# Optimization experiments

Hardware: AMD Instinct MI355X
Metric: run time of the kernel (lower is better)

## Reference

```python
import jax, jax.numpy as jnp
import numpy as np

N_STATE = 64   # n == m (required by the broadcast in the original forward)
SEQ_LEN = 200000


def setup_inputs() -> dict:
    key = jax.random.key(0)
    k_y, k_a, k_h = jax.random.split(key, 3)
    n = N_STATE
    # A scaled so spectral radius ~0.9 (stable recurrence), H ~ O(1) rows
    A = 0.9 * jax.random.normal(k_a, (n, n), dtype=jnp.float32) / jnp.sqrt(jnp.float32(n))
    H = jax.random.normal(k_h, (n, n), dtype=jnp.float32) / jnp.sqrt(jnp.float32(n))
    y = jax.random.normal(k_y, (n, SEQ_LEN), dtype=jnp.float32)
    L = jnp.float32(0.2)  # scalar learned gain (self.weights)
    return {"y": y, "A": A, "H": H, "L": L, "N": SEQ_LEN}


def reference(y, A, H, L, N):
    # x_{k+1} = A x_k + L * (y_k - H x_k);  yhat_k = H x_k  (pre-update state)
    # Vectorized over time with lax.scan (true sequential dependence).
    def step(x, yk):
        out = H @ x                      # [n] observation prediction at step k
        x_next = A @ x + L * (yk - out)  # [n] state update
        return x_next, out

    x0 = jnp.zeros((A.shape[0],), dtype=y.dtype)
    _, yhat_t = jax.lax.scan(step, x0, y.T)  # scan over time axis: y.T is [N, m]
    return yhat_t.T                          # [m, N]
```

## Files before the change

### kernel.cpp

```cpp
#include <hip/hip_runtime.h>


#define CHUNK 64
#define LOOKBACK 8

__global__ __launch_bounds__(1024) void kf_setup(const float* __restrict__ A,
                                                 const float* __restrict__ Hm,
                                                 const float* __restrict__ Lp,
                                                 float* __restrict__ ws) {
  __shared__ __align__(16) float s0[64 * 68];
  __shared__ __align__(16) float s1[64 * 68];
  const float Lg = Lp[0];
  const int t  = threadIdx.x;
  const int r  = t >> 4;
  const int c0 = (t & 15) * 4;

  {
    const float4 a4 = *(const float4*)(A  + r * 64 + c0);
    const float4 h4 = *(const float4*)(Hm + r * 64 + c0);
    float4 m4;
    m4.x = fmaf(-Lg, h4.x, a4.x);
    m4.y = fmaf(-Lg, h4.y, a4.y);
    m4.z = fmaf(-Lg, h4.z, a4.z);
    m4.w = fmaf(-Lg, h4.w, a4.w);
    *(float4*)(s0 + r * 68 + c0) = m4;
  }
  __syncthreads();

  float* src = s0;
  float* dst = s1;
  for (int sq = 0; sq < 6; ++sq) {
    float4 acc = make_float4(0.f, 0.f, 0.f, 0.f);
    const float* srow = src + r * 68;
    #pragma unroll 8
    for (int k = 0; k < 64; ++k) {
      const float  a  = srow[k];
      const float4 b4 = *(const float4*)(src + k * 68 + c0);
      acc.x = fmaf(a, b4.x, acc.x);
      acc.y = fmaf(a, b4.y, acc.y);
      acc.z = fmaf(a, b4.z, acc.z);
      acc.w = fmaf(a, b4.w, acc.w);
    }
    __syncthreads();
    *(float4*)(dst + r * 68 + c0) = acc;
    __syncthreads();
    float* tmp = src; src = dst; dst = tmp;
  }
  *(float4*)(ws + r * 64 + c0) = *(const float4*)(src + r * 68 + c0);
}

__global__ __launch_bounds__(64, 1) void kf_phase1(const float* __restrict__ y,
                                                   const float* __restrict__ A,
                                                   const float* __restrict__ Hm,
                                                   const float* __restrict__ Lp,
                                                   float* __restrict__ bvec,
                                                   int Nv) {
  const int c    = blockIdx.x;
  const int lane = threadIdx.x;
  const float Lg = Lp[0];
  __shared__ __align__(16) float xs[64];

  float Mrow[64];
  {
    const float* Ar = A  + lane * 64;
    const float* Hr = Hm + lane * 64;
    #pragma unroll
    for (int j = 0; j < 64; j += 4) {
      const float4 a4 = *(const float4*)(Ar + j);
      const float4 h4 = *(const float4*)(Hr + j);
      Mrow[j + 0] = fmaf(-Lg, h4.x, a4.x);
      Mrow[j + 1] = fmaf(-Lg, h4.y, a4.y);
      Mrow[j + 2] = fmaf(-Lg, h4.z, a4.z);
      Mrow[j + 3] = fmaf(-Lg, h4.w, a4.w);
    }
  }

  const int k0 = c * CHUNK;
  const float* yrow = y + (size_t)lane * (size_t)Nv + k0;
  const int nst = min(CHUNK, Nv - k0);
  float x = 0.f;

  if (nst == CHUNK) {
    #pragma unroll 1
    for (int t = 0; t < 4; ++t) {
      const float4 y0 = *(const float4*)(yrow + 16 * t + 0);
      const float4 y1 = *(const float4*)(yrow + 16 * t + 4);
      const float4 y2 = *(const float4*)(yrow + 16 * t + 8);
      const float4 y3 = *(const float4*)(yrow + 16 * t + 12);
      float yb[16];
      yb[0] = y0.x; yb[1] = y0.y; yb[2]  = y0.z; yb[3]  = y0.w;
      yb[4] = y1.x; yb[5] = y1.y; yb[6]  = y1.z; yb[7]  = y1.w;
      yb[8] = y2.x; yb[9] = y2.y; yb[10] = y2.z; yb[11] = y2.w;
      yb[12] = y3.x; yb[13] = y3.y; yb[14] = y3.z; yb[15] = y3.w;
      #pragma unroll
      for (int kk = 0; kk < 16; ++kk) {
        xs[lane] = x;
        __syncthreads();
        float a0 = 0.f, a1 = 0.f;
        #pragma unroll
        for (int jj = 0; jj < 16; ++jj) {
          const float4 xv = ((const float4*)xs)[jj];
          a0 = fmaf(Mrow[4 * jj + 0], xv.x, a0);
          a1 = fmaf(Mrow[4 * jj + 1], xv.y, a1);
          a0 = fmaf(Mrow[4 * jj + 2], xv.z, a0);
          a1 = fmaf(Mrow[4 * jj + 3], xv.w, a1);
        }
        __syncthreads();
        x = fmaf(Lg, yb[kk], a0 + a1);
      }
    }
  } else {
    for (int kk = 0; kk < nst; ++kk) {
      xs[lane] = x;
      __syncthreads();
      float a0 = 0.f, a1 = 0.f;
      #pragma unroll
      for (int jj = 0; jj < 16; ++jj) {
        const float4 xv = ((const float4*)xs)[jj];
        a0 = fmaf(Mrow[4 * jj + 0], xv.x, a0);
        a1 = fmaf(Mrow[4 * jj + 1], xv.y, a1);
        a0 = fmaf(Mrow[4 * jj + 2], xv.z, a0);
        a1 = fmaf(Mrow[4 * jj + 3], xv.w, a1);
      }
      __syncthreads();
      x = fmaf(Lg, yrow[kk], a0 + a1);
    }
  }
  bvec[c * 64 + lane] = x;
}

__global__ __launch_bounds__(64, 1) void kf_phase3(const float* __restrict__ y,
                                                   const float* __restrict__ A,
                                                   const float* __restrict__ Hm,
                                                   const float* __restrict__ Lp,
                                                   const float* __restrict__ bvec,
                                                   const float* __restrict__ P64,
                                                   float* __restrict__ out,
                                                   int Nv) {
  const int c    = blockIdx.x;
  const int lane = threadIdx.x;
  const float Lg = Lp[0];
  __shared__ __align__(16) float xs[64];

  float Mrow[64];
  {
    const float* Ar = A  + lane * 64;
    const float* Hr = Hm + lane * 64;
    #pragma unroll
    for (int j = 0; j < 64; j += 4) {
      const float4 a4 = *(const float4*)(Ar + j);
      const float4 h4 = *(const float4*)(Hr + j);
      Mrow[j + 0] = fmaf(-Lg, h4.x, a4.x);
      Mrow[j + 1] = fmaf(-Lg, h4.y, a4.y);
      Mrow[j + 2] = fmaf(-Lg, h4.z, a4.z);
      Mrow[j + 3] = fmaf(-Lg, h4.w, a4.w);
    }
  }

  float x = 0.f;
  {
    const int D = min(c, LOOKBACK);
    if (D > 0) {
      float Prow[64];
      #pragma unroll
      for (int j = 0; j < 64; j += 4) {
        const float4 p4 = *(const float4*)(P64 + lane * 64 + j);
        Prow[j + 0] = p4.x; Prow[j + 1] = p4.y;
        Prow[j + 2] = p4.z; Prow[j + 3] = p4.w;
      }
      x = bvec[(c - D) * 64 + lane];
      for (int t = D - 1; t >= 1; --t) {
        xs[lane] = x;
        __syncthreads();
        float a0 = 0.f, a1 = 0.f;
        #pragma unroll
        for (int jj = 0; jj < 16; ++jj) {
          const float4 xv = ((const float4*)xs)[jj];
          a0 = fmaf(Prow[4 * jj + 0], xv.x, a0);
          a1 = fmaf(Prow[4 * jj + 1], xv.y, a1);
          a0 = fmaf(Prow[4 * jj + 2], xv.z, a0);
          a1 = fmaf(Prow[4 * jj + 3], xv.w, a1);
        }
        __syncthreads();
        x = a0 + a1 + bvec[(c - t) * 64 + lane];
      }
    }
  }

  float Hrow[64];
  #pragma unroll
  for (int j = 0; j < 64; j += 4) {
    const float4 h4 = *(const float4*)(Hm + lane * 64 + j);
    Hrow[j + 0] = h4.x; Hrow[j + 1] = h4.y;
    Hrow[j + 2] = h4.z; Hrow[j + 3] = h4.w;
  }

  const int k0 = c * CHUNK;
  const float* yrow = y   + (size_t)lane * (size_t)Nv + k0;
  float*       orow = out + (size_t)lane * (size_t)Nv + k0;
  const int nst = min(CHUNK, Nv - k0);

  if (nst == CHUNK) {
    #pragma unroll 1
    for (int t = 0; t < 4; ++t) {
      const float4 y0 = *(const float4*)(yrow + 16 * t + 0);
      const float4 y1 = *(const float4*)(yrow + 16 * t + 4);
      const float4 y2 = *(const float4*)(yrow + 16 * t + 8);
      const float4 y3 = *(const float4*)(yrow + 16 * t + 12);
      float yb[16];
      yb[0] = y0.x; yb[1] = y0.y; yb[2]  = y0.z; yb[3]  = y0.w;
      yb[4] = y1.x; yb[5] = y1.y; yb[6]  = y1.z; yb[7]  = y1.w;
      yb[8] = y2.x; yb[9] = y2.y; yb[10] = y2.z; yb[11] = y2.w;
      yb[12] = y3.x; yb[13] = y3.y; yb[14] = y3.z; yb[15] = y3.w;

      float ob[16];
      #pragma unroll
      for (int kk = 0; kk < 16; ++kk) {
        xs[lane] = x;
        __syncthreads();
        float h0 = 0.f, h1 = 0.f, m0 = 0.f, m1 = 0.f;
        #pragma unroll
        for (int jj = 0; jj < 16; ++jj) {
          const float4 xv = ((const float4*)xs)[jj];
          h0 = fmaf(Hrow[4 * jj + 0], xv.x, h0);
          h1 = fmaf(Hrow[4 * jj + 1], xv.y, h1);
          m0 = fmaf(Mrow[4 * jj + 0], xv.x, m0);
          m1 = fmaf(Mrow[4 * jj + 1], xv.y, m1);
          h0 = fmaf(Hrow[4 * jj + 2], xv.z, h0);
          h1 = fmaf(Hrow[4 * jj + 3], xv.w, h1);
          m0 = fmaf(Mrow[4 * jj + 2], xv.z, m0);
          m1 = fmaf(Mrow[4 * jj + 3], xv.w, m1);
        }
        __syncthreads();
        ob[kk] = h0 + h1;
        x = fmaf(Lg, yb[kk], m0 + m1);
      }
      *(float4*)(orow + 16 * t + 0)  = make_float4(ob[0],  ob[1],  ob[2],  ob[3]);
      *(float4*)(orow + 16 * t + 4)  = make_float4(ob[4],  ob[5],  ob[6],  ob[7]);
      *(float4*)(orow + 16 * t + 8)  = make_float4(ob[8],  ob[9],  ob[10], ob[11]);
      *(float4*)(orow + 16 * t + 12) = make_float4(ob[12], ob[13], ob[14], ob[15]);
    }
  } else {
    for (int kk = 0; kk < nst; ++kk) {
      xs[lane] = x;
      __syncthreads();
      float h0 = 0.f, h1 = 0.f, m0 = 0.f, m1 = 0.f;
      #pragma unroll
      for (int jj = 0; jj < 16; ++jj) {
        const float4 xv = ((const float4*)xs)[jj];
        h0 = fmaf(Hrow[4 * jj + 0], xv.x, h0);
        h1 = fmaf(Hrow[4 * jj + 1], xv.y, h1);
        m0 = fmaf(Mrow[4 * jj + 0], xv.x, m0);
        m1 = fmaf(Mrow[4 * jj + 1], xv.y, m1);
        h0 = fmaf(Hrow[4 * jj + 2], xv.z, h0);
        h1 = fmaf(Hrow[4 * jj + 3], xv.w, h1);
        m0 = fmaf(Mrow[4 * jj + 2], xv.z, m0);
        m1 = fmaf(Mrow[4 * jj + 3], xv.w, m1);
      }
      __syncthreads();
      orow[kk] = h0 + h1;
      x = fmaf(Lg, yrow[kk], m0 + m1);
    }
  }
}

extern "C" void kernel_launch(void* const* d_in, const int* in_sizes, int n_in,
                              void* d_out, int out_size, void* d_ws, size_t ws_size,
                              hipStream_t stream) {
  const float* y  = (const float*)d_in[0];
  const float* A  = (const float*)d_in[1];
  const float* Hm = (const float*)d_in[2];
  const float* Lp = (const float*)d_in[3];
  const int Nv = in_sizes[0] / 64;
  const int P  = (Nv + CHUNK - 1) / CHUNK;

  float* ws   = (float*)d_ws;
  float* P64  = ws;
  float* bvec = ws + 4096;

  kf_setup<<<1, 1024, 0, stream>>>(A, Hm, Lp, P64);
  kf_phase1<<<P, 64, 0, stream>>>(y, A, Hm, Lp, bvec, Nv);
  kf_phase3<<<P, 64, 0, stream>>>(y, A, Hm, Lp, bvec, P64, (float*)d_out, Nv);
}
```

Before: 319.6 us.

## Batch several time chunks per block and zero-pad lookback to drop branches

Phase 1 now runs four independent chunks per 64-thread block and phase 3 runs two, packing their states into a float4 or float2 in shared memory. One barrier pair and one shared-memory read of the state then serve several chunks, which cuts the number of blocks and amortises synchronisation latency. The setup kernel zeros eight padding chunks ahead of the b-vector buffer, so the lookback always runs a fixed eight steps without a D<LOOKBACK branch. The partial-chunk tail path is gone, so correctness now depends on the sequence length being a multiple of the chunk size, and each step does more FMAs per thread.

```diff
diff --git a/kernel.cpp b/kernel.cpp
--- a/kernel.cpp
+++ b/kernel.cpp
@@ -14,6 +14,8 @@
   const int t  = threadIdx.x;
   const int r  = t >> 4;
   const int c0 = (t & 15) * 4;
+
+  if (t < 512) ws[4096 + t] = 0.f;
 
   {
     const float4 a4 = *(const float4*)(A  + r * 64 + c0);
@@ -53,12 +55,12 @@
                                                    const float* __restrict__ A,
                                                    const float* __restrict__ Hm,
                                                    const float* __restrict__ Lp,
-                                                   float* __restrict__ bvec,
-                                                   int Nv) {
-  const int c    = blockIdx.x;
+                                                   float* __restrict__ bb,
+                                                   int Nv, int P) {
   const int lane = threadIdx.x;
+  const int cb   = blockIdx.x * 4;
   const float Lg = Lp[0];
-  __shared__ __align__(16) float xs[64];
+  __shared__ __align__(16) float4 xs[64];
 
   float Mrow[64];
   {
@@ -75,72 +77,72 @@
     }
   }
 
-  const int k0 = c * CHUNK;
-  const float* yrow = y + (size_t)lane * (size_t)Nv + k0;
-  const int nst = min(CHUNK, Nv - k0);
-  float x = 0.f;
-
-  if (nst == CHUNK) {
-    #pragma unroll 1
-    for (int t = 0; t < 4; ++t) {
-      const float4 y0 = *(const float4*)(yrow + 16 * t + 0);
-      const float4 y1 = *(const float4*)(yrow + 16 * t + 4);
-      const float4 y2 = *(const float4*)(yrow + 16 * t + 8);
-      const float4 y3 = *(const float4*)(yrow + 16 * t + 12);
-      float yb[16];
-      yb[0] = y0.x; yb[1] = y0.y; yb[2]  = y0.z; yb[3]  = y0.w;
-      yb[4] = y1.x; yb[5] = y1.y; yb[6]  = y1.z; yb[7]  = y1.w;
-      yb[8] = y2.x; yb[9] = y2.y; yb[10] = y2.z; yb[11] = y2.w;
-      yb[12] = y3.x; yb[13] = y3.y; yb[14] = y3.z; yb[15] = y3.w;
+  const int c0 = min(cb + 0, P - 1);
+  const int c1 = min(cb + 1, P - 1);
+  const int c2 = min(cb + 2, P - 1);
+  const int c3 = min(cb + 3, P - 1);
+  const float* y0 = y + (size_t)lane * (size_t)Nv + c0 * CHUNK;
+  const float* y1 = y + (size_t)lane * (size_t)Nv + c1 * CHUNK;
+  const float* y2 = y + (size_t)lane * (size_t)Nv + c2 * CHUNK;
+  const float* y3 = y + (size_t)lane * (size_t)Nv + c3 * CHUNK;
+
+  float x0 = 0.f, x1 = 0.f, x2 = 0.f, x3 = 0.f;
+
+  #pragma unroll 1
+  for (int t = 0; t < 8; ++t) {
+    const float4 pa0 = *(const float4*)(y0 + 8 * t);
+    const float4 pb0 = *(const float4*)(y0 + 8 * t + 4);
+    const float4 pa1 = *(const float4*)(y1 + 8 * t);
+    const float4 pb1 = *(const float4*)(y1 + 8 * t + 4);
+    const float4 pa2 = *(const float4*)(y2 + 8 * t);
+    const float4 pb2 = *(const float4*)(y2 + 8 * t + 4);
+    const float4 pa3 = *(const float4*)(y3 + 8 * t);
+    const float4 pb3 = *(const float4*)(y3 + 8 * t + 4);
+    float yb0[8] = {pa0.x, pa0.y, pa0.z, pa0.w, pb0.x, pb0.y, pb0.z, pb0.w};
+    float yb1[8] = {pa1.x, pa1.y, pa1.z, pa1.w, pb1.x, pb1.y, pb1.z, pb1.w};
+    float yb2[8] = {pa2.x, pa2.y, pa2.z, pa2.w, pb2.x, pb2.y, pb2.z, pb2.w};
+    float yb3[8] = {pa3.x, pa3.y, pa3.z, pa3.w, pb3.x, pb3.y, pb3.z, pb3.w};
+
+    #pragma unroll
+    for (int kk = 0; kk < 8; ++kk) {
+      xs[lane] = make_float4(x0, x1, x2, x3);
+      __syncthreads();
+      float a0 = 0.f, a1 = 0.f, a2 = 0.f, a3 = 0.f;
       #pragma unroll
-      for (int kk = 0; kk < 16; ++kk) {
-        xs[lane] = x;
-        __syncthreads();
-        float a0 = 0.f, a1 = 0.f;
-        #pragma unroll
-        for (int jj = 0; jj < 16; ++jj) {
-          const float4 xv = ((const float4*)xs)[jj];
-          a0 = fmaf(Mrow[4 * jj + 0], xv.x, a0);
-          a1 = fmaf(Mrow[4 * jj + 1], xv.y, a1);
-          a0 = fmaf(Mrow[4 * jj + 2], xv.z, a0);
-          a1 = fmaf(Mrow[4 * jj + 3], xv.w, a1);
-        }
-        __syncthreads();
-        x = fmaf(Lg, yb[kk], a0 + a1);
+      for (int j = 0; j < 64; ++j) {
+        const float4 v = xs[j];
+        a0 = fmaf(Mrow[j], v.x, a0);
+        a1 = fmaf(Mrow[j], v.y, a1);
+        a2 = fmaf(Mrow[j], v.z, a2);
+        a3 = fmaf(Mrow[j], v.w, a3);
       }
-    }
-  } else {
-    for (int kk = 0; kk < nst; ++kk) {
-      xs[lane] = x;
-      __syncthreads();
-      float a0 = 0.f, a1 = 0.f;
-      #pragma unroll
-      for (int jj = 0; jj < 16; ++jj) {
-        const float4 xv = ((const float4*)xs)[jj];
-        a0 = fmaf(Mrow[4 * jj + 0], xv.x, a0);
-        a1 = fmaf(Mrow[4 * jj + 1], xv.y, a1);
-        a0 = fmaf(Mrow[4 * jj + 2], xv.z, a0);
-        a1 = fmaf(Mrow[4 * jj + 3], xv.w, a1);
-      }
-      __syncthreads();
-      x = fmaf(Lg, yrow[kk], a0 + a1);
-    }
-  }
-  bvec[c * 64 + lane] = x;
+      __syncthreads();
+      x0 = fmaf(Lg, yb0[kk], a0);
+      x1 = fmaf(Lg, yb1[kk], a1);
+      x2 = fmaf(Lg, yb2[kk], a2);
+      x3 = fmaf(Lg, yb3[kk], a3);
+    }
+  }
+  bb[c0 * 64 + lane] = x0;
+  bb[c1 * 64 + lane] = x1;
+  bb[c2 * 64 + lane] = x2;
+  bb[c3 * 64 + lane] = x3;
 }
 
 __global__ __launch_bounds__(64, 1) void kf_phase3(const float* __restrict__ y,
                                                    const float* __restrict__ A,
                                                    const float* __restrict__ Hm,
                                                    const float* __restrict__ Lp,
-                                                   const float* __restrict__ bvec,
+                                                   const float* __restrict__ bb,
                                                    const float* __restrict__ P64,
                                                    float* __restrict__ out,
-                                                   int Nv) {
-  const int c    = blockIdx.x;
+                                                   int Nv, int P) {
   const int lane = threadIdx.x;
+  const int cb   = blockIdx.x * 2;
+  const int c0   = min(cb + 0, P - 1);
+  const int c1   = min(cb + 1, P - 1);
   const float Lg = Lp[0];
-  __shared__ __align__(16) float xs[64];
+  __shared__ __align__(16) float2 xs[64];
 
   float Mrow[64];
   {
@@ -157,33 +159,33 @@
     }
   }
 
-  float x = 0.f;
-  {
-    const int D = min(c, LOOKBACK);
-    if (D > 0) {
-      float Prow[64];
+  float x0, x1;
+  {
+    float Prow[64];
+    #pragma unroll
+    for (int j = 0; j < 64; j += 4) {
+      const float4 p4 = *(const float4*)(P64 + lane * 64 + j);
+      Prow[j + 0] = p4.x; Prow[j + 1] = p4.y;
+      Prow[j + 2] = p4.z; Prow[j + 3] = p4.w;
+    }
+    x0 = bb[(c0 - LOOKBACK) * 64 + lane];
+    x1 = bb[(c1 - LOOKBACK) * 64 + lane];
+    #pragma unroll 1
+    for (int t = LOOKBACK - 1; t >= 1; --t) {
+      xs[lane] = make_float2(x0, x1);
+      __syncthreads();
+      float p0 = 0.f, p1 = 0.f, q0 = 0.f, q1 = 0.f;
       #pragma unroll
-      for (int j = 0; j < 64; j += 4) {
-        const float4 p4 = *(const float4*)(P64 + lane * 64 + j);
-        Prow[j + 0] = p4.x; Prow[j + 1] = p4.y;
-        Prow[j + 2] = p4.z; Prow[j + 3] = p4.w;
+      for (int jj = 0; jj < 32; ++jj) {
+        const float4 v = ((const float4*)xs)[jj];
+        p0 = fmaf(Prow[2 * jj + 0], v.x, p0);
+        p1 = fmaf(Prow[2 * jj + 0], v.y, p1);
+        q0 = fmaf(Prow[2 * jj + 1], v.z, q0);
+        q1 = fmaf(Prow[2 * jj + 1], v.w, q1);
       }
-      x = bvec[(c - D) * 64 + lane];
-      for (int t = D - 1; t >= 1; --t) {
-        xs[lane] = x;
-        __syncthreads();
-        float a0 = 0.f, a1 = 0.f;
-        #pragma unroll
-        for (int jj = 0; jj < 16; ++jj) {
-          const float4 xv = ((const float4*)xs)[jj];
-          a0 = fmaf(Prow[4 * jj + 0], xv.x, a0);
-          a1 = fmaf(Prow[4 * jj + 1], xv.y, a1);
-          a0 = fmaf(Prow[4 * jj + 2], xv.z, a0);
-          a1 = fmaf(Prow[4 * jj + 3], xv.w, a1);
-        }
-        __syncthreads();
-        x = a0 + a1 + bvec[(c - t) * 64 + lane];
-      }
+      __syncthreads();
+      x0 = p0 + q0 + bb[(c0 - t) * 64 + lane];
+      x1 = p1 + q1 + bb[(c1 - t) * 64 + lane];
     }
   }
 
@@ -195,72 +197,49 @@
     Hrow[j + 2] = h4.z; Hrow[j + 3] = h4.w;
   }
 
-  const int k0 = c * CHUNK;
-  const float* yrow = y   + (size_t)lane * (size_t)Nv + k0;
-  float*       orow = out + (size_t)lane * (size_t)Nv + k0;
-  const int nst = min(CHUNK, Nv - k0);
-
-  if (nst == CHUNK) {
-    #pragma unroll 1
-    for (int t = 0; t < 4; ++t) {
-      const float4 y0 = *(const float4*)(yrow + 16 * t + 0);
-      const float4 y1 = *(const float4*)(yrow + 16 * t + 4);
-      const float4 y2 = *(const float4*)(yrow + 16 * t + 8);
-      const float4 y3 = *(const float4*)(yrow + 16 * t + 12);
-      float yb[16];
-      yb[0] = y0.x; yb[1] = y0.y; yb[2]  = y0.z; yb[3]  = y0.w;
-      yb[4] = y1.x; yb[5] = y1.y; yb[6]  = y1.z; yb[7]  = y1.w;
-      yb[8] = y2.x; yb[9] = y2.y; yb[10] = y2.z; yb[11] = y2.w;
-      yb[12] = y3.x; yb[13] = y3.y; yb[14] = y3.z; yb[15] = y3.w;
-
-      float ob[16];
+  const float* yr0 = y   + (size_t)lane * (size_t)Nv + c0 * CHUNK;
+  const float* yr1 = y   + (size_t)lane * (size_t)Nv + c1 * CHUNK;
+  float*       o0  = out + (size_t)lane * (size_t)Nv + c0 * CHUNK;
+  float*       o1  = out + (size_t)lane * (size_t)Nv + c1 * CHUNK;
+
+  #pragma unroll 1
+  for (int t = 0; t < 8; ++t) {
+    const float4 pa0 = *(const float4*)(yr0 + 8 * t);
+    const float4 pb0 = *(const float4*)(yr0 + 8 * t + 4);
+    const float4 pa1 = *(const float4*)(yr1 + 8 * t);
+    const float4 pb1 = *(const float4*)(yr1 + 8 * t + 4);
+    float yb0[8] = {pa0.x, pa0.y, pa0.z, pa0.w, pb0.x, pb0.y, pb0.z, pb0.w};
+    float yb1[8] = {pa1.x, pa1.y, pa1.z, pa1.w, pb1.x, pb1.y, pb1.z, pb1.w};
+    float ob0[8], ob1[8];
+
+    #pragma unroll
+    for (int kk = 0; kk < 8; ++kk) {
+      xs[lane] = make_float2(x0, x1);
+      __syncthreads();
+      float h0e = 0.f, h1e = 0.f, m0e = 0.f, m1e = 0.f;
+      float h0o = 0.f, h1o = 0.f, m0o = 0.f, m1o = 0.f;
       #pragma unroll
-      for (int kk = 0; kk < 16; ++kk) {
-        xs[lane] = x;
-        __syncthreads();
-        float h0 = 0.f, h1 = 0.f, m0 = 0.f, m1 = 0.f;
-        #pragma unroll
-        for (int jj = 0; jj < 16; ++jj) {
-          const float4 xv = ((const float4*)xs)[jj];
-          h0 = fmaf(Hrow[4 * jj + 0], xv.x, h0);
-          h1 = fmaf(Hrow[4 * jj + 1], xv.y, h1);
-          m0 = fmaf(Mrow[4 * jj + 0], xv.x, m0);
-          m1 = fmaf(Mrow[4 * jj + 1], xv.y, m1);
-          h0 = fmaf(Hrow[4 * jj + 2], xv.z, h0);
-          h1 = fmaf(Hrow[4 * jj + 3], xv.w, h1);
-          m0 = fmaf(Mrow[4 * jj + 2], xv.z, m0);
-          m1 = fmaf(Mrow[4 * jj + 3], xv.w, m1);
-        }
-        __syncthreads();
-        ob[kk] = h0 + h1;
-        x = fmaf(Lg, yb[kk], m0 + m1);
+      for (int jj = 0; jj < 32; ++jj) {
+        const float4 v = ((const float4*)xs)[jj];
+        h0e = fmaf(Hrow[2 * jj + 0], v.x, h0e);
+        h1e = fmaf(Hrow[2 * jj + 0], v.y, h1e);
+        m0e = fmaf(Mrow[2 * jj + 0], v.x, m0e);
+        m1e = fmaf(Mrow[2 * jj + 0], v.y, m1e);
+        h0o = fmaf(Hrow[2 * jj + 1], v.z, h0o);
+        h1o = fmaf(Hrow[2 * jj + 1], v.w, h1o);
+        m0o = fmaf(Mrow[2 * jj + 1], v.z, m0o);
+        m1o = fmaf(Mrow[2 * jj + 1], v.w, m1o);
       }
-      *(float4*)(orow + 16 * t + 0)  = make_float4(ob[0],  ob[1],  ob[2],  ob[3]);
-      *(float4*)(orow + 16 * t + 4)  = make_float4(ob[4],  ob[5],  ob[6],  ob[7]);
-      *(float4*)(orow + 16 * t + 8)  = make_float4(ob[8],  ob[9],  ob[10], ob[11]);
-      *(float4*)(orow + 16 * t + 12) = make_float4(ob[12], ob[13], ob[14], ob[15]);
-    }
-  } else {
-    for (int kk = 0; kk < nst; ++kk) {
-      xs[lane] = x;
-      __syncthreads();
-      float h0 = 0.f, h1 = 0.f, m0 = 0.f, m1 = 0.f;
-      #pragma unroll
-      for (int jj = 0; jj < 16; ++jj) {
-        const float4 xv = ((const float4*)xs)[jj];
-        h0 = fmaf(Hrow[4 * jj + 0], xv.x, h0);
-        h1 = fmaf(Hrow[4 * jj + 1], xv.y, h1);
-        m0 = fmaf(Mrow[4 * jj + 0], xv.x, m0);
-        m1 = fmaf(Mrow[4 * jj + 1], xv.y, m1);
-        h0 = fmaf(Hrow[4 * jj + 2], xv.z, h0);
-        h1 = fmaf(Hrow[4 * jj + 3], xv.w, h1);
-        m0 = fmaf(Mrow[4 * jj + 2], xv.z, m0);
-        m1 = fmaf(Mrow[4 * jj + 3], xv.w, m1);
-      }
-      __syncthreads();
-      orow[kk] = h0 + h1;
-      x = fmaf(Lg, yrow[kk], m0 + m1);
-    }
+      __syncthreads();
+      ob0[kk] = h0e + h0o;
+      ob1[kk] = h1e + h1o;
+      x0 = fmaf(Lg, yb0[kk], m0e + m0o);
+      x1 = fmaf(Lg, yb1[kk], m1e + m1o);
+    }
+    *(float4*)(o0 + 8 * t)     = make_float4(ob0[0], ob0[1], ob0[2], ob0[3]);
+    *(float4*)(o0 + 8 * t + 4) = make_float4(ob0[4], ob0[5], ob0[6], ob0[7]);
+    *(float4*)(o1 + 8 * t)     = make_float4(ob1[0], ob1[1], ob1[2], ob1[3]);
+    *(float4*)(o1 + 8 * t + 4) = make_float4(ob1[4], ob1[5], ob1[6], ob1[7]);
   }
 }
 
@@ -276,9 +255,9 @@
 
   float* ws   = (float*)d_ws;
   float* P64  = ws;
-  float* bvec = ws + 4096;
-
-  kf_setup<<<1, 1024, 0, stream>>>(A, Hm, Lp, P64);
-  kf_phase1<<<P, 64, 0, stream>>>(y, A, Hm, Lp, bvec, Nv);
-  kf_phase3<<<P, 64, 0, stream>>>(y, A, Hm, Lp, bvec, P64, (float*)d_out, Nv);
-}
+  float* bb   = ws + 4096 + 512;
+
+  kf_setup<<<1, 1024, 0, stream>>>(A, Hm, Lp, ws);
+  kf_phase1<<<(P + 3) / 4, 64, 0, stream>>>(y, A, Hm, Lp, bb, Nv, P);
+  kf_phase3<<<(P + 1) / 2, 64, 0, stream>>>(y, A, Hm, Lp, bb, P64, (float*)d_out, Nv, P);
+}
```

Result: slower. 871.5 us (+172.7%).

## Replace LDS broadcast and barriers with readlane broadcasts in recurrence loops

Applied to the files above, without the earlier changes.

The per-step state broadcast now uses wave readlane intrinsics instead of an LDS store, two __syncthreads and LDS loads, since each block is a single 64-lane wavefront. Each step then runs as pure register/scalar work. The lookback branch is removed by zero-padding 8 chunks of bvec ahead of the real data, so every block runs a uniform lookback. Launch bounds are raised to allow more blocks per CU, and accumulation is split into four chains for more ILP. Readlane puts 64 scalar ops on the critical path of every step, and the higher occupancy target may cost registers.

```diff
diff --git a/kernel.cpp b/kernel.cpp
--- a/kernel.cpp
+++ b/kernel.cpp
@@ -3,6 +3,10 @@
 
 #define CHUNK 64
 #define LOOKBACK 8
+
+__device__ __forceinline__ float bcast(float x, int l) {
+  return __uint_as_float(__builtin_amdgcn_readlane(__float_as_uint(x), l));
+}
 
 __global__ __launch_bounds__(1024) void kf_setup(const float* __restrict__ A,
                                                  const float* __restrict__ Hm,
@@ -14,6 +18,8 @@
   const int t  = threadIdx.x;
   const int r  = t >> 4;
   const int c0 = (t & 15) * 4;
+
+  if (t < 512) ws[4096 + t] = 0.f;
 
   {
     const float4 a4 = *(const float4*)(A  + r * 64 + c0);
@@ -49,16 +55,15 @@
   *(float4*)(ws + r * 64 + c0) = *(const float4*)(src + r * 68 + c0);
 }
 
-__global__ __launch_bounds__(64, 1) void kf_phase1(const float* __restrict__ y,
+__global__ __launch_bounds__(64, 4) void kf_phase1(const float* __restrict__ y,
                                                    const float* __restrict__ A,
                                                    const float* __restrict__ Hm,
                                                    const float* __restrict__ Lp,
-                                                   float* __restrict__ bvec,
+                                                   float* __restrict__ bb,
                                                    int Nv) {
   const int c    = blockIdx.x;
   const int lane = threadIdx.x;
   const float Lg = Lp[0];
-  __shared__ __align__(16) float xs[64];
 
   float Mrow[64];
   {
@@ -82,65 +87,58 @@
 
   if (nst == CHUNK) {
     #pragma unroll 1
-    for (int t = 0; t < 4; ++t) {
-      const float4 y0 = *(const float4*)(yrow + 16 * t + 0);
-      const float4 y1 = *(const float4*)(yrow + 16 * t + 4);
-      const float4 y2 = *(const float4*)(yrow + 16 * t + 8);
-      const float4 y3 = *(const float4*)(yrow + 16 * t + 12);
-      float yb[16];
-      yb[0] = y0.x; yb[1] = y0.y; yb[2]  = y0.z; yb[3]  = y0.w;
-      yb[4] = y1.x; yb[5] = y1.y; yb[6]  = y1.z; yb[7]  = y1.w;
-      yb[8] = y2.x; yb[9] = y2.y; yb[10] = y2.z; yb[11] = y2.w;
-      yb[12] = y3.x; yb[13] = y3.y; yb[14] = y3.z; yb[15] = y3.w;
-      #pragma unroll
-      for (int kk = 0; kk < 16; ++kk) {
-        xs[lane] = x;
-        __syncthreads();
-        float a0 = 0.f, a1 = 0.f;
+    for (int t = 0; t < 8; ++t) {
+      const float4 p0 = *(const float4*)(yrow + 8 * t);
+      const float4 p1 = *(const float4*)(yrow + 8 * t + 4);
+      const float yb[8] = {p0.x, p0.y, p0.z, p0.w, p1.x, p1.y, p1.z, p1.w};
+      #pragma unroll
+      for (int kk = 0; kk < 8; ++kk) {
+        float a0 = 0.f, a1 = 0.f, a2 = 0.f, a3 = 0.f;
         #pragma unroll
-        for (int jj = 0; jj < 16; ++jj) {
-          const float4 xv = ((const float4*)xs)[jj];
-          a0 = fmaf(Mrow[4 * jj + 0], xv.x, a0);
-          a1 = fmaf(Mrow[4 * jj + 1], xv.y, a1);
-          a0 = fmaf(Mrow[4 * jj + 2], xv.z, a0);
-          a1 = fmaf(Mrow[4 * jj + 3], xv.w, a1);
+        for (int j = 0; j < 64; j += 4) {
+          const float s0 = bcast(x, j + 0);
+          const float s1 = bcast(x, j + 1);
+          const float s2 = bcast(x, j + 2);
+          const float s3 = bcast(x, j + 3);
+          a0 = fmaf(Mrow[j + 0], s0, a0);
+          a1 = fmaf(Mrow[j + 1], s1, a1);
+          a2 = fmaf(Mrow[j + 2], s2, a2);
+          a3 = fmaf(Mrow[j + 3], s3, a3);
         }
-        __syncthreads();
-        x = fmaf(Lg, yb[kk], a0 + a1);
+        x = fmaf(Lg, yb[kk], (a0 + a1) + (a2 + a3));
       }
     }
   } else {
     for (int kk = 0; kk < nst; ++kk) {
-      xs[lane] = x;
-      __syncthreads();
-      float a0 = 0.f, a1 = 0.f;
-      #pragma unroll
-      for (int jj = 0; jj < 16; ++jj) {
-        const float4 xv = ((const float4*)xs)[jj];
-        a0 = fmaf(Mrow[4 * jj + 0], xv.x, a0);
-        a1 = fmaf(Mrow[4 * jj + 1], xv.y, a1);
-        a0 = fmaf(Mrow[4 * jj + 2], xv.z, a0);
-        a1 = fmaf(Mrow[4 * jj + 3], xv.w, a1);
-      }
-      __syncthreads();
-      x = fmaf(Lg, yrow[kk], a0 + a1);
-    }
-  }
-  bvec[c * 64 + lane] = x;
-}
-
-__global__ __launch_bounds__(64, 1) void kf_phase3(const float* __restrict__ y,
+      float a0 = 0.f, a1 = 0.f, a2 = 0.f, a3 = 0.f;
+      #pragma unroll
+      for (int j = 0; j < 64; j += 4) {
+        const float s0 = bcast(x, j + 0);
+        const float s1 = bcast(x, j + 1);
+        const float s2 = bcast(x, j + 2);
+        const float s3 = bcast(x, j + 3);
+        a0 = fmaf(Mrow[j + 0], s0, a0);
+        a1 = fmaf(Mrow[j + 1], s1, a1);
+        a2 = fmaf(Mrow[j + 2], s2, a2);
+        a3 = fmaf(Mrow[j + 3], s3, a3);
+      }
+      x = fmaf(Lg, yrow[kk], (a0 + a1) + (a2 + a3));
+    }
+  }
+  bb[c * 64 + lane] = x;
+}
+
+__global__ __launch_bounds__(64, 2) void kf_phase3(const float* __restrict__ y,
                                                    const float* __restrict__ A,
                                                    const float* __restrict__ Hm,
                                                    const float* __restrict__ Lp,
-                                                   const float* __restrict__ bvec,
+                                                   const float* __restrict__ bb,
                                                    const float* __restrict__ P64,
                                                    float* __restrict__ out,
                                                    int Nv) {
   const int c    = blockIdx.x;
   const int lane = threadIdx.x;
   const float Lg = Lp[0];
-  __shared__ __align__(16) float xs[64];
 
   float Mrow[64];
   {
@@ -157,33 +155,31 @@
     }
   }
 
-  float x = 0.f;
-  {
-    const int D = min(c, LOOKBACK);
-    if (D > 0) {
-      float Prow[64];
+  float x;
+  {
+    float Prow[64];
+    #pragma unroll
+    for (int j = 0; j < 64; j += 4) {
+      const float4 p4 = *(const float4*)(P64 + lane * 64 + j);
+      Prow[j + 0] = p4.x; Prow[j + 1] = p4.y;
+      Prow[j + 2] = p4.z; Prow[j + 3] = p4.w;
+    }
+    x = bb[(c - LOOKBACK) * 64 + lane];
+    #pragma unroll 1
+    for (int t = LOOKBACK - 1; t >= 1; --t) {
+      float a0 = 0.f, a1 = 0.f, a2 = 0.f, a3 = 0.f;
       #pragma unroll
       for (int j = 0; j < 64; j += 4) {
-        const float4 p4 = *(const float4*)(P64 + lane * 64 + j);
-        Prow[j + 0] = p4.x; Prow[j + 1] = p4.y;
-        Prow[j + 2] = p4.z; Prow[j + 3] = p4.w;
-      }
-      x = bvec[(c - D) * 64 + lane];
-      for (int t = D - 1; t >= 1; --t) {
-        xs[lane] = x;
-        __syncthreads();
-        float a0 = 0.f, a1 = 0.f;
-        #pragma unroll
-        for (int jj = 0; jj < 16; ++jj) {
-          const float4 xv = ((const float4*)xs)[jj];
-          a0 = fmaf(Prow[4 * jj + 0], xv.x, a0);
-          a1 = fmaf(Prow[4 * jj + 1], xv.y, a1);
-          a0 = fmaf(Prow[4 * jj + 2], xv.z, a0);
-          a1 = fmaf(Prow[4 * jj + 3], xv.w, a1);
-        }
-        __syncthreads();
-        x = a0 + a1 + bvec[(c - t) * 64 + lane];
-      }
+        const float s0 = bcast(x, j + 0);
+        const float s1 = bcast(x, j + 1);
+        const float s2 = bcast(x, j + 2);
+        const float s3 = bcast(x, j + 3);
+        a0 = fmaf(Prow[j + 0], s0, a0);
+        a1 = fmaf(Prow[j + 1], s1, a1);
+        a2 = fmaf(Prow[j + 2], s2, a2);
+        a3 = fmaf(Prow[j + 3], s3, a3);
+      }
+      x = (a0 + a1) + (a2 + a3) + bb[(c - t) * 64 + lane];
     }
   }
 
@@ -202,64 +198,57 @@
 
   if (nst == CHUNK) {
     #pragma unroll 1
-    for (int t = 0; t < 4; ++t) {
-      const float4 y0 = *(const float4*)(yrow + 16 * t + 0);
-      const float4 y1 = *(const float4*)(yrow + 16 * t + 4);
-      const float4 y2 = *(const float4*)(yrow + 16 * t + 8);
-      const float4 y3 = *(const float4*)(yrow + 16 * t + 12);
-      float yb[16];
-      yb[0] = y0.x; yb[1] = y0.y; yb[2]  = y0.z; yb[3]  = y0.w;
-      yb[4] = y1.x; yb[5] = y1.y; yb[6]  = y1.z; yb[7]  = y1.w;
-      yb[8] = y2.x; yb[9] = y2.y; yb[10] = y2.z; yb[11] = y2.w;
-      yb[12] = y3.x; yb[13] = y3.y; yb[14] = y3.z; yb[15] = y3.w;
-
-      float ob[16];
-      #pragma unroll
-      for (int kk = 0; kk < 16; ++kk) {
-        xs[lane] = x;
-        __syncthreads();
-        float h0 = 0.f, h1 = 0.f, m0 = 0.f, m1 = 0.f;
+    for (int t = 0; t < 8; ++t) {
+      const float4 p0 = *(const float4*)(yrow + 8 * t);
+      const float4 p1 = *(const float4*)(yrow + 8 * t + 4);
+      const float yb[8] = {p0.x, p0.y, p0.z, p0.w, p1.x, p1.y, p1.z, p1.w};
+      float ob[8];
+      #pragma unroll
+      for (int kk = 0; kk < 8; ++kk) {
+        float h0 = 0.f, h1 = 0.f, h2 = 0.f, h3 = 0.f;
+        float m0 = 0.f, m1 = 0.f, m2 = 0.f, m3 = 0.f;
         #pragma unroll
-        for (int jj = 0; jj < 16; ++jj) {
-          const float4 xv = ((const float4*)xs)[jj];
-          h0 = fmaf(Hrow[4 * jj + 0], xv.x, h0);
-          h1 = fmaf(Hrow[4 * jj + 1], xv.y, h1);
-          m0 = fmaf(Mrow[4 * jj + 0], xv.x, m0);
-          m1 = fmaf(Mrow[4 * jj + 1], xv.y, m1);
-          h0 = fmaf(Hrow[4 * jj + 2], xv.z, h0);
-          h1 = fmaf(Hrow[4 * jj + 3], xv.w, h1);
-          m0 = fmaf(Mrow[4 * jj + 2], xv.z, m0);
-          m1 = fmaf(Mrow[4 * jj + 3], xv.w, m1);
+        for (int j = 0; j < 64; j += 4) {
+          const float s0 = bcast(x, j + 0);
+          const float s1 = bcast(x, j + 1);
+          const float s2 = bcast(x, j + 2);
+          const float s3 = bcast(x, j + 3);
+          h0 = fmaf(Hrow[j + 0], s0, h0);
+          m0 = fmaf(Mrow[j + 0], s0, m0);
+          h1 = fmaf(Hrow[j + 1], s1, h1);
+          m1 = fmaf(Mrow[j + 1], s1, m1);
+          h2 = fmaf(Hrow[j + 2], s2, h2);
+          m2 = fmaf(Mrow[j + 2], s2, m2);
+          h3 = fmaf(Hrow[j + 3], s3, h3);
+          m3 = fmaf(Mrow[j + 3], s3, m3);
         }
-        __syncthreads();
-        ob[kk] = h0 + h1;
-        x = fmaf(Lg, yb[kk], m0 + m1);
-      }
-      *(float4*)(orow + 16 * t + 0)  = make_float4(ob[0],  ob[1],  ob[2],  ob[3]);
-      *(float4*)(orow + 16 * t + 4)  = make_float4(ob[4],  ob[5],  ob[6],  ob[7]);
-      *(float4*)(orow + 16 * t + 8)  = make_float4(ob[8],  ob[9],  ob[10], ob[11]);
-      *(float4*)(orow + 16 * t + 12) = make_float4(ob[12], ob[13], ob[14], ob[15]);
+        ob[kk] = (h0 + h1) + (h2 + h3);
+        x = fmaf(Lg, yb[kk], (m0 + m1) + (m2 + m3));
+      }
+      *(float4*)(orow + 8 * t)     = make_float4(ob[0], ob[1], ob[2], ob[3]);
+      *(float4*)(orow + 8 * t + 4) = make_float4(ob[4], ob[5], ob[6], ob[7]);
     }
   } else {
     for (int kk = 0; kk < nst; ++kk) {
-      xs[lane] = x;
-      __syncthreads();
-      float h0 = 0.f, h1 = 0.f, m0 = 0.f, m1 = 0.f;
-      #pragma unroll
-      for (int jj = 0; jj < 16; ++jj) {
-        const float4 xv = ((const float4*)xs)[jj];
-        h0 = fmaf(Hrow[4 * jj + 0], xv.x, h0);
-        h1 = fmaf(Hrow[4 * jj + 1], xv.y, h1);
-        m0 = fmaf(Mrow[4 * jj + 0], xv.x, m0);
-        m1 = fmaf(Mrow[4 * jj + 1], xv.y, m1);
-        h0 = fmaf(Hrow[4 * jj + 2], xv.z, h0);
-        h1 = fmaf(Hrow[4 * jj + 3], xv.w, h1);
-        m0 = fmaf(Mrow[4 * jj + 2], xv.z, m0);
-        m1 = fmaf(Mrow[4 * jj + 3], xv.w, m1);
-      }
-      __syncthreads();
-      orow[kk] = h0 + h1;
-      x = fmaf(Lg, yrow[kk], m0 + m1);
+      float h0 = 0.f, h1 = 0.f, h2 = 0.f, h3 = 0.f;
+      float m0 = 0.f, m1 = 0.f, m2 = 0.f, m3 = 0.f;
+      #pragma unroll
+      for (int j = 0; j < 64; j += 4) {
+        const float s0 = bcast(x, j + 0);
+        const float s1 = bcast(x, j + 1);
+        const float s2 = bcast(x, j + 2);
+        const float s3 = bcast(x, j + 3);
+        h0 = fmaf(Hrow[j + 0], s0, h0);
+        m0 = fmaf(Mrow[j + 0], s0, m0);
+        h1 = fmaf(Hrow[j + 1], s1, h1);
+        m1 = fmaf(Mrow[j + 1], s1, m1);
+        h2 = fmaf(Hrow[j + 2], s2, h2);
+        m2 = fmaf(Mrow[j + 2], s2, m2);
+        h3 = fmaf(Hrow[j + 3], s3, h3);
+        m3 = fmaf(Mrow[j + 3], s3, m3);
+      }
+      orow[kk] = (h0 + h1) + (h2 + h3);
+      x = fmaf(Lg, yrow[kk], (m0 + m1) + (m2 + m3));
     }
   }
 }
@@ -276,9 +265,9 @@
 
   float* ws   = (float*)d_ws;
   float* P64  = ws;
-  float* bvec = ws + 4096;
-
-  kf_setup<<<1, 1024, 0, stream>>>(A, Hm, Lp, P64);
-  kf_phase1<<<P, 64, 0, stream>>>(y, A, Hm, Lp, bvec, Nv);
-  kf_phase3<<<P, 64, 0, stream>>>(y, A, Hm, Lp, bvec, P64, (float*)d_out, Nv);
-}
+  float* bb   = ws + 4096 + 512;
+
+  kf_setup<<<1, 1024, 0, stream>>>(A, Hm, Lp, ws);
+  kf_phase1<<<P, 64, 0, stream>>>(y, A, Hm, Lp, bb, Nv);
+  kf_phase3<<<P, 64, 0, stream>>>(y, A, Hm, Lp, bb, P64, (float*)d_out, Nv);
+}
```

Result: faster. 263.4 us (-17.6%).
